# Optimization experiments

Hardware: AMD Instinct MI355X
Metric: run time of the kernel (lower is better)

The kernel has to match this reference:

```python
import jax, jax.numpy as jnp
import numpy as np

B, C, F = 8192, 2048, 2048


def setup_inputs() -> dict:
    key = jax.random.key(0)
    k1, k2 = jax.random.split(key)
    x = jax.random.normal(k1, (B, F), dtype=jnp.float32)
    means = jax.random.normal(k2, (C, F), dtype=jnp.float32)
    # scalar 'variance' parameter used as a divisor (std); realistic post-update value
    variance = jnp.ones((1,), dtype=jnp.float32)
    return {"x": x, "means": means, "variance": variance}


def reference(x, means, variance):
    # non-deep_nno, eval-mode branch: x = x / std with std = variance param
    xs = x / variance  # [B, F]
    # L2 distance to class means via GEMM cdist: ||a-b|| = sqrt(||a||^2 + ||b||^2 - 2 a.b)
    x2 = jnp.sum(xs * xs, axis=1, keepdims=True)          # [B, 1]
    m2 = jnp.sum(means * means, axis=1)                    # [C]
    cross = jnp.einsum('bf,cf->bc', xs, means)             # [B, C] GEMM
    d2 = jnp.maximum(x2 + m2[None, :] - 2.0 * cross, 0.0)  # clamp fp error
    cumulative_diff = jnp.sqrt(d2)                         # torch.norm(diff, p=2, dim=2)
    exponent = -cumulative_diff
    probs = jax.nn.softmax(exponent, axis=1)
    return (probs, exponent, cumulative_diff)
```

## Files before the change

kernel.cpp:

```cpp
#include <hip/hip_runtime.h>
#include <hip/hip_bf16.h>

constexpr int BB = 8192;
constexpr int CC = 2048;
constexpr int FF = 2048;

typedef __bf16 bf16x8 __attribute__((ext_vector_type(8)));
typedef float  f32x4  __attribute__((ext_vector_type(4)));

typedef __attribute__((address_space(1))) unsigned int gu32;
typedef __attribute__((address_space(3))) unsigned int lu32;

__device__ __forceinline__ void async_copy16(const void* g, void* l) {
    __builtin_amdgcn_global_load_lds(
        (gu32*)(unsigned long long)g,
        (lu32*)(unsigned int)(unsigned long long)l,
        16, 0, 0);
}

__global__ void prep_rows(const float* __restrict__ in,
                          unsigned short* __restrict__ outb,
                          float* __restrict__ sq,
                          const float* __restrict__ varp) {
    const int row = blockIdx.x;
    const int t = threadIdx.x;
    const float scale = varp ? (1.0f / varp[0]) : 1.0f;
    const size_t base = (size_t)row * FF + (size_t)t * 8;
    const float4 a = *(const float4*)(in + base);
    const float4 b = *(const float4*)(in + base + 4);
    float v[8] = {a.x * scale, a.y * scale, a.z * scale, a.w * scale,
                  b.x * scale, b.y * scale, b.z * scale, b.w * scale};
    float s = 0.0f;
    bf16x8 h;
#pragma unroll
    for (int i = 0; i < 8; ++i) {
        s += v[i] * v[i];
        h[i] = (__bf16)v[i];
    }
    *(bf16x8*)(outb + base) = h;
#pragma unroll
    for (int off = 32; off > 0; off >>= 1) s += __shfl_down(s, off);
    __shared__ float red[4];
    if ((t & 63) == 0) red[t >> 6] = s;
    __syncthreads();
    if (t == 0) sq[row] = (red[0] + red[1]) + (red[2] + red[3]);
}

__global__ __launch_bounds__(256, 2) void gemm_epi(
    const unsigned short* __restrict__ A,
    const unsigned short* __restrict__ Bm,
    const float* __restrict__ x2,
    const float* __restrict__ m2,
    float* __restrict__ expo,
    float* __restrict__ cum) {
    __shared__ __align__(16) unsigned short As[128 * 32];
    __shared__ __align__(16) unsigned short Bs[128 * 32];

    const int t = threadIdx.x;
    const int wave = t >> 6, lane = t & 63;
    const int bx = blockIdx.x;
    const int bm = bx & 63;
    const int bn = bx >> 6;
    const int wm = wave >> 1, wn = wave & 1;
    const int rowA0 = bm * 128, rowB0 = bn * 128;

    const int srow = lane >> 2;
    const int scol = (lane & 3) * 8;

    const int ar = wm * 64 + (lane & 15);
    const int br = wn * 64 + (lane & 15);
    const int kk = (lane >> 4) * 8;

    f32x4 acc[4][4] = {};

    for (int k0 = 0; k0 < FF; k0 += 32) {
#pragma unroll
        for (int r = 0; r < 2; ++r) {
            const int chunk = r * 4 + wave;
            const int rr = chunk * 16 + srow;
            async_copy16(&A[(size_t)(rowA0 + rr) * FF + k0 + scol], &As[chunk * 512]);
            async_copy16(&Bm[(size_t)(rowB0 + rr) * FF + k0 + scol], &Bs[chunk * 512]);
        }
        __syncthreads();

        bf16x8 af[4], bf[4];
#pragma unroll
        for (int i = 0; i < 4; ++i) af[i] = *(const bf16x8*)&As[(ar + i * 16) * 32 + kk];
#pragma unroll
        for (int j = 0; j < 4; ++j) bf[j] = *(const bf16x8*)&Bs[(br + j * 16) * 32 + kk];
#pragma unroll
        for (int i = 0; i < 4; ++i)
#pragma unroll
            for (int j = 0; j < 4; ++j)
                acc[i][j] = __builtin_amdgcn_mfma_f32_16x16x32_bf16(af[i], bf[j], acc[i][j], 0, 0, 0);
        __syncthreads();
    }

    const int ln = lane & 15, lq = lane >> 4;
    const int grow0 = rowA0 + wm * 64 + lq * 4;
    const int gcol0 = rowB0 + wn * 64 + ln;
    float x2v[16];
#pragma unroll
    for (int i = 0; i < 4; ++i)
#pragma unroll
        for (int r = 0; r < 4; ++r) x2v[i * 4 + r] = x2[grow0 + i * 16 + r];
    float m2v[4];
#pragma unroll
    for (int j = 0; j < 4; ++j) m2v[j] = m2[gcol0 + j * 16];

#pragma unroll
    for (int i = 0; i < 4; ++i)
#pragma unroll
        for (int j = 0; j < 4; ++j)
#pragma unroll
            for (int r = 0; r < 4; ++r) {
                const float d2 = x2v[i * 4 + r] + m2v[j] - 2.0f * acc[i][j][r];
                const float d = sqrtf(fmaxf(d2, 0.0f));
                const size_t idx = (size_t)(grow0 + i * 16 + r) * CC + (gcol0 + j * 16);
                cum[idx] = d;
                expo[idx] = -d;
            }
}

__global__ void softmax_rows(const float* __restrict__ e, float* __restrict__ p) {
    const int row = blockIdx.x;
    const int t = threadIdx.x;
    const size_t base = (size_t)row * CC + (size_t)t * 8;
    const float4 a = *(const float4*)(e + base);
    const float4 b = *(const float4*)(e + base + 4);
    float v[8] = {a.x, a.y, a.z, a.w, b.x, b.y, b.z, b.w};

    float mx = v[0];
#pragma unroll
    for (int i = 1; i < 8; ++i) mx = fmaxf(mx, v[i]);
#pragma unroll
    for (int off = 32; off > 0; off >>= 1) mx = fmaxf(mx, __shfl_down(mx, off));
    __shared__ float redm[4], reds[4];
    if ((t & 63) == 0) redm[t >> 6] = mx;
    __syncthreads();
    mx = fmaxf(fmaxf(redm[0], redm[1]), fmaxf(redm[2], redm[3]));

    float ev[8];
    float s = 0.0f;
#pragma unroll
    for (int i = 0; i < 8; ++i) {
        ev[i] = __expf(v[i] - mx);
        s += ev[i];
    }
#pragma unroll
    for (int off = 32; off > 0; off >>= 1) s += __shfl_down(s, off);
    if ((t & 63) == 0) reds[t >> 6] = s;
    __syncthreads();
    s = (reds[0] + reds[1]) + (reds[2] + reds[3]);
    const float inv = 1.0f / s;

    float4 o0 = {ev[0] * inv, ev[1] * inv, ev[2] * inv, ev[3] * inv};
    float4 o1 = {ev[4] * inv, ev[5] * inv, ev[6] * inv, ev[7] * inv};
    *(float4*)(p + base) = o0;
    *(float4*)(p + base + 4) = o1;
}

extern "C" void kernel_launch(void* const* d_in, const int* in_sizes, int n_in,
                              void* d_out, int out_size, void* d_ws, size_t ws_size,
                              hipStream_t stream) {
    const float* x     = (const float*)d_in[0];
    const float* means = (const float*)d_in[1];
    const float* var   = (const float*)d_in[2];
    float* out = (float*)d_out;

    unsigned short* xb = (unsigned short*)d_ws;
    unsigned short* mb = xb + (size_t)BB * FF;
    float* x2 = (float*)(mb + (size_t)CC * FF);
    float* m2 = x2 + BB;

    float* probs = out;
    float* expo  = out + (size_t)BB * CC;
    float* cum   = expo + (size_t)BB * CC;

    prep_rows<<<BB, 256, 0, stream>>>(x, xb, x2, var);
    prep_rows<<<CC, 256, 0, stream>>>(means, mb, m2, nullptr);
    gemm_epi<<<(BB / 128) * (CC / 128), 256, 0, stream>>>(xb, mb, x2, m2, expo, cum);
    softmax_rows<<<BB, 256, 0, stream>>>(expo, probs);
}
```

Baseline: 359.7 us.

## Swizzle LDS tiles, group block order, merge prep launches, nontemporal stores

Applies an XOR swizzle to the LDS column layout of the A and B tiles so the fragment reads avoid bank conflicts. Remaps block indices into groups of 8 row-tiles sharing column tiles, for better L2 reuse. Merges the two prep launches into one and writes the cum output with nontemporal stores so it does not pollute the cache that softmax needs for expo. Several unrelated tweaks change together, and the swizzle must agree between the async write side and the read side.

```diff
diff --git a/kernel.cpp b/kernel.cpp
--- a/kernel.cpp
+++ b/kernel.cpp
@@ -18,13 +18,20 @@
         16, 0, 0);
 }
 
-__global__ void prep_rows(const float* __restrict__ in,
-                          unsigned short* __restrict__ outb,
-                          float* __restrict__ sq,
+__global__ void prep_rows(const float* __restrict__ x,
+                          const float* __restrict__ means,
+                          unsigned short* __restrict__ xb,
+                          unsigned short* __restrict__ mb,
+                          float* __restrict__ x2,
+                          float* __restrict__ m2,
                           const float* __restrict__ varp) {
-    const int row = blockIdx.x;
+    const int blk = blockIdx.x;
+    const bool isx = blk < BB;
+    const int row = isx ? blk : blk - BB;
     const int t = threadIdx.x;
-    const float scale = varp ? (1.0f / varp[0]) : 1.0f;
+    const float scale = isx ? (1.0f / varp[0]) : 1.0f;
+    const float* in = isx ? x : means;
+    unsigned short* outb = isx ? xb : mb;
     const size_t base = (size_t)row * FF + (size_t)t * 8;
     const float4 a = *(const float4*)(in + base);
     const float4 b = *(const float4*)(in + base + 4);
@@ -43,7 +50,10 @@
     __shared__ float red[4];
     if ((t & 63) == 0) red[t >> 6] = s;
     __syncthreads();
-    if (t == 0) sq[row] = (red[0] + red[1]) + (red[2] + red[3]);
+    if (t == 0) {
+        float tot = (red[0] + red[1]) + (red[2] + red[3]);
+        if (isx) x2[row] = tot; else m2[row] = tot;
+    }
 }
 
 __global__ __launch_bounds__(256, 2) void gemm_epi(
@@ -59,17 +69,18 @@
     const int t = threadIdx.x;
     const int wave = t >> 6, lane = t & 63;
     const int bx = blockIdx.x;
-    const int bm = bx & 63;
-    const int bn = bx >> 6;
+    const int bm = ((bx >> 7) << 3) | (bx & 7);
+    const int bn = (bx >> 3) & 15;
     const int wm = wave >> 1, wn = wave & 1;
     const int rowA0 = bm * 128, rowB0 = bn * 128;
 
     const int srow = lane >> 2;
-    const int scol = (lane & 3) * 8;
+    const int scol = (((lane & 3) ^ ((lane >> 3) & 3))) * 8;
 
-    const int ar = wm * 64 + (lane & 15);
-    const int br = wn * 64 + (lane & 15);
-    const int kk = (lane >> 4) * 8;
+    const int rl = lane & 15;
+    const int kphys = (((lane >> 4) ^ ((rl >> 1) & 3))) * 8;
+    const int ar = wm * 64 + rl;
+    const int br = wn * 64 + rl;
 
     f32x4 acc[4][4] = {};
 
@@ -85,9 +96,9 @@
 
         bf16x8 af[4], bf[4];
 #pragma unroll
-        for (int i = 0; i < 4; ++i) af[i] = *(const bf16x8*)&As[(ar + i * 16) * 32 + kk];
+        for (int i = 0; i < 4; ++i) af[i] = *(const bf16x8*)&As[(ar + i * 16) * 32 + kphys];
 #pragma unroll
-        for (int j = 0; j < 4; ++j) bf[j] = *(const bf16x8*)&Bs[(br + j * 16) * 32 + kk];
+        for (int j = 0; j < 4; ++j) bf[j] = *(const bf16x8*)&Bs[(br + j * 16) * 32 + kphys];
 #pragma unroll
         for (int i = 0; i < 4; ++i)
 #pragma unroll
@@ -117,7 +128,7 @@
                 const float d2 = x2v[i * 4 + r] + m2v[j] - 2.0f * acc[i][j][r];
                 const float d = sqrtf(fmaxf(d2, 0.0f));
                 const size_t idx = (size_t)(grow0 + i * 16 + r) * CC + (gcol0 + j * 16);
-                cum[idx] = d;
+                __builtin_nontemporal_store(d, &cum[idx]);
                 expo[idx] = -d;
             }
 }
@@ -177,8 +188,7 @@
     float* expo  = out + (size_t)BB * CC;
     float* cum   = expo + (size_t)BB * CC;
 
-    prep_rows<<<BB, 256, 0, stream>>>(x, xb, x2, var);
-    prep_rows<<<CC, 256, 0, stream>>>(means, mb, m2, nullptr);
+    prep_rows<<<BB + CC, 256, 0, stream>>>(x, means, xb, mb, x2, m2, var);
     gemm_epi<<<(BB / 128) * (CC / 128), 256, 0, stream>>>(xb, mb, x2, m2, expo, cum);
     softmax_rows<<<BB, 256, 0, stream>>>(expo, probs);
 }
```

Measured after the change: 349.7 us. -2.8%, faster.
